# Kernel optimization log

Measured on AMD Instinct MI355X. Metric: run time of the kernel, lower is better.

## Reference

```python
import jax, jax.numpy as jnp
import numpy as np

B, S_IMG, S_TXT, D, H, HD = 1, 2048, 512, 3072, 24, 128
EMB, N_IP = 4096, 64
IP_SCALE = 1.0
EPS = 1e-6
SM_SCALE = 1.0 / np.sqrt(HD).astype(np.float32)


def _lin(x, W, b=None):
    # torch Linear: y = x @ W.T + b, W: [out, in]
    y = jnp.einsum('bsd,od->bso', x, W)
    return y if b is None else y + b


def _heads(x):  # [B,S,D] -> [B,H,S,HD]
    return x.reshape(B, -1, H, HD).transpose(0, 2, 1, 3)


def _rms(x, w):
    return x * jax.lax.rsqrt(jnp.mean(x * x, axis=-1, keepdims=True) + EPS) * w


def _rope(x, cos, sin):
    # interleaved real/imag rotation, cos/sin: [S, HD] broadcast over B,H
    xr = x.reshape(*x.shape[:-1], HD // 2, 2)
    rot = jnp.stack([-xr[..., 1], xr[..., 0]], axis=-1).reshape(x.shape)
    return x * cos + rot * sin


def _sdpa(q, k, v):
    s = jnp.einsum('bhqd,bhkd->bhqk', q, k) * SM_SCALE
    p = jax.nn.softmax(s, axis=-1)
    return jnp.einsum('bhqk,bhkd->bhqd', p, v)


def setup_inputs() -> dict:
    key = jax.random.key(0)
    ks = jax.random.split(key, 32)
    r = lambda i, shape: jax.random.normal(ks[i], shape, dtype=jnp.float32)
    w = lambda i, shape: r(i, shape) * 0.02
    inp = {
        'hidden_states': r(0, (B, S_IMG, D)),
        'encoder_hidden_states': r(1, (B, S_TXT, D)),
        'image_embeds': r(2, (B, N_IP, EMB)),
        'rope_cos': jnp.cos(r(3, (S_TXT + S_IMG, HD))),
        'rope_sin': jnp.sin(r(3, (S_TXT + S_IMG, HD))),
        'Wq': w(4, (D, D)), 'bq': jnp.zeros((D,)),
        'Wk': w(5, (D, D)), 'bk': jnp.zeros((D,)),
        'Wv': w(6, (D, D)), 'bv': jnp.zeros((D,)),
        'Waq': w(7, (D, D)), 'baq': jnp.zeros((D,)),
        'Wak': w(8, (D, D)), 'bak': jnp.zeros((D,)),
        'Wav': w(9, (D, D)), 'bav': jnp.zeros((D,)),
        'Wo': w(10, (D, D)), 'bo': jnp.zeros((D,)),
        'Wao': w(11, (D, D)), 'bao': jnp.zeros((D,)),
        'norm_q_w': jnp.ones((HD,)), 'norm_k_w': jnp.ones((HD,)),
        'norm_aq_w': jnp.ones((HD,)), 'norm_ak_w': jnp.ones((HD,)),
        'Wk_ip': w(12, (D, EMB)), 'Wv_ip': w(13, (D, EMB)),
        'txt_seq_len': S_TXT,
    }
    return inp


def reference(hidden_states, encoder_hidden_states, image_embeds, rope_cos, rope_sin,
              Wq, bq, Wk, bk, Wv, bv, Waq, baq, Wak, bak, Wav, bav,
              Wo, bo, Wao, bao, norm_q_w, norm_k_w, norm_aq_w, norm_ak_w,
              Wk_ip, Wv_ip, txt_seq_len):
    # main stream projections + per-head RMSNorm
    q = _rms(_heads(_lin(hidden_states, Wq, bq)), norm_q_w)
    k = _rms(_heads(_lin(hidden_states, Wk, bk)), norm_k_w)
    v = _heads(_lin(hidden_states, Wv, bv))
    # encoder (text) stream projections + RMSNorm, concat text before image
    eq = _rms(_heads(_lin(encoder_hidden_states, Waq, baq)), norm_aq_w)
    ek = _rms(_heads(_lin(encoder_hidden_states, Wak, bak)), norm_ak_w)
    ev = _heads(_lin(encoder_hidden_states, Wav, bav))
    q = jnp.concatenate([eq, q], axis=2)
    k = jnp.concatenate([ek, k], axis=2)
    v = jnp.concatenate([ev, v], axis=2)
    # IP-adapter branch uses pre-RoPE image-token queries
    ip_q = q[:, :, txt_seq_len:]
    ip_k = _heads(_lin(image_embeds, Wk_ip))
    ip_v = _heads(_lin(image_embeds, Wv_ip))
    ip_hs = _sdpa(ip_q, ip_k, ip_v).transpose(0, 2, 1, 3).reshape(B, -1, H * HD)
    # rotary on joint q/k, then main attention
    q = _rope(q, rope_cos, rope_sin)
    k = _rope(k, rope_cos, rope_sin)
    hs = _sdpa(q, k, v).transpose(0, 2, 1, 3).reshape(B, -1, H * HD)
    # add scaled IP-adapter output to the image part
    img = hs[:, txt_seq_len:] + IP_SCALE * ip_hs
    enc = hs[:, :txt_seq_len]
    # output projections
    out_img = _lin(img, Wo, bo)
    out_enc = _lin(enc, Wao, bao)
    return out_img, out_enc
```

## Files before the change

### kernel.cpp

```cpp
#include <hip/hip_runtime.h>
#include <hip/hip_bf16.h>

#define H 24
#define HD 128
#define DMODEL 3072
#define S_IMG 2048
#define S_TXT 512
#define S_ALL 2560
#define EMB 4096
#define N_IP 64
#define SM_SCALE 0.08838834764831845f

typedef __attribute__((ext_vector_type(8))) short short8;
typedef __attribute__((ext_vector_type(4))) float f32x4;
typedef __attribute__((ext_vector_type(16))) float f32x16;

__device__ inline unsigned short f2bf(float f) {
    unsigned u = __builtin_bit_cast(unsigned, f);
    return (unsigned short)((u + 0x7fffu + ((u >> 16) & 1u)) >> 16);
}
__device__ inline unsigned pk2(float a, float b) {
    return (unsigned)f2bf(a) | ((unsigned)f2bf(b) << 16);
}
__device__ inline float bf2f(unsigned short u) {
    unsigned x = ((unsigned)u) << 16;
    return __builtin_bit_cast(float, x);
}

__device__ inline void gload16(const void* g, void* l) {
    __builtin_amdgcn_global_load_lds(
        (const __attribute__((address_space(1))) unsigned int*)g,
        (__attribute__((address_space(3))) unsigned int*)(unsigned int)(unsigned long long)l,
        16, 0, 0);
}

struct CastSegs {
    const float* src[13];
    unsigned short* dst[13];
    int n8[13];
    int ntot8[13];
    int bstart[14];
};

__global__ __launch_bounds__(256)
void castall(CastSegs cs)
{
    int b = blockIdx.x, seg = 0;
    while (seg < 12 && b >= cs.bstart[seg + 1]) seg++;
    int nb = cs.bstart[seg + 1] - cs.bstart[seg];
    int lb = b - cs.bstart[seg];
    const float* in = cs.src[seg];
    unsigned short* out = cs.dst[seg];
    int n8 = cs.n8[seg], ntot = cs.ntot8[seg];
    for (int i = lb * 256 + threadIdx.x; i < ntot; i += nb * 256) {
        int4 o;
        if (i < n8) {
            const float4* p = (const float4*)(in + (size_t)i * 8);
            float4 a = p[0], bb = p[1];
            o.x = pk2(a.x, a.y); o.y = pk2(a.z, a.w);
            o.z = pk2(bb.x, bb.y); o.w = pk2(bb.z, bb.w);
        } else {
            o.x = 0; o.y = 0; o.z = 0; o.w = 0;
        }
        *(int4*)(out + (size_t)i * 8) = o;
    }
}

__global__ __launch_bounds__(256)
void bcat2(const float* __restrict__ q0, const float* __restrict__ k0, const float* __restrict__ v0,
           const float* __restrict__ q1, const float* __restrict__ k1, const float* __restrict__ v1,
           float* __restrict__ d0, float* __restrict__ d1)
{
    int i = blockIdx.x * 256 + threadIdx.x;
    int which = i >= 3 * DMODEL;
    int j = which ? i - 3 * DMODEL : i;
    const float* a = which ? q1 : q0;
    const float* b = which ? k1 : k0;
    const float* c = which ? v1 : v0;
    float v = (j < DMODEL) ? a[j] : ((j < 2 * DMODEL) ? b[j - DMODEL] : c[j - 2 * DMODEL]);
    (which ? d1 : d0)[j] = v;
}

template<int OUTBF>
__global__ __launch_bounds__(256)
void gemmx(const unsigned short* __restrict__ A0, const unsigned short* __restrict__ B0,
           const float* __restrict__ b0, void* __restrict__ C0,
           const unsigned short* __restrict__ A1, const unsigned short* __restrict__ B1,
           const float* __restrict__ b1, void* __restrict__ C1,
           int mbSplit, int N, int K, int nbm, int GN)
{
    __shared__ unsigned short sm[2 * 8192];
    const int tid = threadIdx.x, lane = tid & 63, wid = tid >> 6;
    const int wr = wid >> 1, wc = wid & 1;
    const int r15 = lane & 15, g = lane >> 4;

    int nwg = gridDim.x;
    int t = (blockIdx.x & 7) * (nwg >> 3) + (blockIdx.x >> 3);
    int gsz = nbm * GN;
    int G = t / gsz, l = t - G * gsz;
    int mb = l % nbm, nb = G * GN + l / nbm;

    const unsigned short* A; const unsigned short* B; const float* bias; void* C; int mrow;
    if (mb < mbSplit) { A = A0; B = B0; bias = b0; C = C0; mrow = mb; }
    else             { A = A1; B = B1; bias = b1; C = C1; mrow = mb - mbSplit; }
    const int m0 = mrow * 128, n0 = nb * 128;

    const int lr = lane >> 3;
    const int lc = lane & 7;
    const int gcol = ((lc * 16) ^ (lr << 4)) >> 1;

    const unsigned short* Ab = A + (size_t)(m0 + wid * 32 + lr) * K + gcol;
    const unsigned short* Bb = B + (size_t)(n0 + wid * 32 + lr) * K + gcol;
    char* smc = (char*)sm;

    f32x4 acc[4][4];
    #pragma unroll
    for (int i = 0; i < 4; i++)
        #pragma unroll
        for (int j = 0; j < 4; j++)
            acc[i][j] = {0.f, 0.f, 0.f, 0.f};

    for (int k0 = 0; k0 < K; k0 += 64) {
        #pragma unroll
        for (int cc = 0; cc < 4; cc++) {
            gload16(Ab + (size_t)cc * 8 * K + k0, smc + (wid * 32 + cc * 8) * 128);
            gload16(Bb + (size_t)cc * 8 * K + k0, smc + 16384 + (wid * 32 + cc * 8) * 128);
        }
        __syncthreads();
        #pragma unroll
        for (int ks = 0; ks < 2; ks++) {
            short8 af[4], bf[4];
            #pragma unroll
            for (int mi = 0; mi < 4; mi++) {
                int row = wr * 64 + mi * 16 + r15;
                af[mi] = *(const short8*)(smc + row * 128 + ((ks * 64 + g * 16) ^ ((row & 7) << 4)));
            }
            #pragma unroll
            for (int ni = 0; ni < 4; ni++) {
                int row = wc * 64 + ni * 16 + r15;
                bf[ni] = *(const short8*)(smc + 16384 + row * 128 + ((ks * 64 + g * 16) ^ ((row & 7) << 4)));
            }
            #pragma unroll
            for (int mi = 0; mi < 4; mi++)
                #pragma unroll
                for (int ni = 0; ni < 4; ni++)
                    acc[mi][ni] = __builtin_amdgcn_mfma_f32_16x16x32_bf16(af[mi], bf[ni], acc[mi][ni], 0, 0, 0);
        }
        __syncthreads();
    }
    #pragma unroll
    for (int mi = 0; mi < 4; mi++) {
        #pragma unroll
        for (int ni = 0; ni < 4; ni++) {
            int col = n0 + wc * 64 + ni * 16 + r15;
            float bv = bias ? bias[col] : 0.f;
            #pragma unroll
            for (int r = 0; r < 4; r++) {
                int grow = m0 + wr * 64 + mi * 16 + g * 4 + r;
                float v = acc[mi][ni][r] + bv;
                if (OUTBF)
                    ((unsigned short*)C)[(size_t)grow * N + col] = f2bf(v);
                else
                    ((float*)C)[(size_t)grow * N + col] = v;
            }
        }
    }
}

__global__ __launch_bounds__(256)
void rmsropeQK(const unsigned short* __restrict__ qkvb,
               const float* __restrict__ nqw, const float* __restrict__ nkw,
               const float* __restrict__ naqw, const float* __restrict__ nakw,
               const float* __restrict__ cosb, const float* __restrict__ sinb,
               unsigned short* __restrict__ qb, unsigned short* __restrict__ kb,
               unsigned short* __restrict__ ipq)
{
    int wg = blockIdx.x * 4 + (threadIdx.x >> 6);
    int lane = threadIdx.x & 63;
    int s = wg / H, h = wg - s * H;
    const unsigned short* row = qkvb + (size_t)s * (3 * DMODEL);
    unsigned uq = *(const unsigned*)(row + h * HD + lane * 2);
    unsigned uk = *(const unsigned*)(row + DMODEL + h * HD + lane * 2);
    float q0 = bf2f((unsigned short)uq), q1 = bf2f((unsigned short)(uq >> 16));
    float k0 = bf2f((unsigned short)uk), k1 = bf2f((unsigned short)(uk >> 16));
    float sq = q0 * q0 + q1 * q1, sk = k0 * k0 + k1 * k1;
    #pragma unroll
    for (int off = 1; off < 64; off <<= 1) {
        sq += __shfl_xor(sq, off);
        sk += __shfl_xor(sk, off);
    }
    float rq = rsqrtf(sq * (1.f / HD) + 1e-6f) * SM_SCALE;
    float rk = rsqrtf(sk * (1.f / HD) + 1e-6f);
    const float* wq = (s < S_TXT) ? naqw : nqw;
    const float* wk = (s < S_TXT) ? nakw : nkw;
    float xq0 = q0 * rq * wq[lane * 2], xq1 = q1 * rq * wq[lane * 2 + 1];
    float xk0 = k0 * rk * wk[lane * 2], xk1 = k1 * rk * wk[lane * 2 + 1];
    if (s >= S_TXT)
        *(unsigned*)(ipq + (size_t)h * S_IMG * HD + (size_t)(s - S_TXT) * HD + lane * 2) = pk2(xq0, xq1);
    float c0 = cosb[s * HD + lane * 2], c1 = cosb[s * HD + lane * 2 + 1];
    float s0 = sinb[s * HD + lane * 2], s1 = sinb[s * HD + lane * 2 + 1];
    *(unsigned*)(qb + (size_t)h * S_ALL * HD + (size_t)s * HD + lane * 2) =
        pk2(xq0 * c0 - xq1 * s0, xq1 * c1 + xq0 * s1);
    *(unsigned*)(kb + (size_t)h * S_ALL * HD + (size_t)s * HD + lane * 2) =
        pk2(xk0 * c0 - xk1 * s0, xk1 * c1 + xk0 * s1);
}

__global__ __launch_bounds__(256)
void vtrans(const unsigned short* __restrict__ src, int stride,
            unsigned short* __restrict__ vt, int Stot)
{
    __shared__ unsigned short lv[64 * 130];
    int h = blockIdx.y;
    int s0 = blockIdx.x * 64;
    const unsigned short* base = src + (size_t)s0 * stride + h * HD;
    int tid = threadIdx.x;
    #pragma unroll
    for (int i = 0; i < 4; i++) {
        int slot = tid + 256 * i;
        int row = slot >> 4, c = slot & 15;
        int4 v = *(const int4*)(base + (size_t)row * stride + c * 8);
        unsigned* p = (unsigned*)(lv + row * 130 + c * 8);
        p[0] = (unsigned)v.x; p[1] = (unsigned)v.y; p[2] = (unsigned)v.z; p[3] = (unsigned)v.w;
    }
    __syncthreads();
    #pragma unroll
    for (int i = 0; i < 4; i++) {
        int slot = tid + 256 * i;
        int d = slot >> 3, c8 = slot & 7;
        unsigned w0 = lv[(c8 * 8 + 0) * 130 + d] | ((unsigned)lv[(c8 * 8 + 1) * 130 + d] << 16);
        unsigned w1 = lv[(c8 * 8 + 2) * 130 + d] | ((unsigned)lv[(c8 * 8 + 3) * 130 + d] << 16);
        unsigned w2 = lv[(c8 * 8 + 4) * 130 + d] | ((unsigned)lv[(c8 * 8 + 5) * 130 + d] << 16);
        unsigned w3 = lv[(c8 * 8 + 6) * 130 + d] | ((unsigned)lv[(c8 * 8 + 7) * 130 + d] << 16);
        int4 o = {(int)w0, (int)w1, (int)w2, (int)w3};
        *(int4*)(vt + (size_t)(h * HD + d) * Stot + s0 + c8 * 8) = o;
    }
}

__global__ __launch_bounds__(256)
void cast_heads8(const unsigned short* __restrict__ in, unsigned short* __restrict__ out)
{
    int idx = blockIdx.x * 256 + threadIdx.x;
    int s = idx / 384;
    int rem = idx - s * 384;
    int h = rem >> 4, d8 = rem & 15;
    int4 v = *(const int4*)(in + (size_t)s * (2 * DMODEL) + h * HD + d8 * 8);
    *(int4*)(out + ((size_t)h * N_IP + s) * HD + d8 * 8) = v;
}

template<int MODE, int KVBLK>
__global__ __launch_bounds__(512, 2)
void flash4(const unsigned short* __restrict__ Q, const unsigned short* __restrict__ Kb,
            const unsigned short* __restrict__ Vt, const unsigned short* __restrict__ ipb,
            unsigned short* __restrict__ Out, int Sq, int Skv)
{
    __shared__ char sm[66560];
    const int h = blockIdx.y;
    const int q0 = blockIdx.x * 256;
    const int tid = threadIdx.x, w = tid >> 6, lane = tid & 63;
    const int l31 = lane & 31, hi = lane >> 5;
    const int T2 = KVBLK / 32, K4 = KVBLK / 16, SLOTV = KVBLK / 8, NL = KVBLK / 32;
    const int VROWB = KVBLK * 2;

    const unsigned short* Qh = Q + ((size_t)h * Sq + q0 + w * 32 + l31) * HD + hi * 8;
    short8 qf[8];
    #pragma unroll
    for (int c = 0; c < 8; c++)
        qf[c] = *(const short8*)(Qh + c * 16);

    float m = -3.0e38f, lsum = 0.f;
    f32x16 o[4];
    #pragma unroll
    for (int dn = 0; dn < 4; dn++)
        #pragma unroll
        for (int r = 0; r < 16; r++) o[dn][r] = 0.f;

    const unsigned short* Kh = Kb + (size_t)h * Skv * HD;
    const unsigned short* Vth = Vt + (size_t)h * HD * Skv;
    float* scl = (float*)(sm + 65536) + w * 32;
    const int nt = Skv / KVBLK;

    for (int t = 0; t < nt; t++) {
        int kv0 = t * KVBLK;
        #pragma unroll
        for (int cc = 0; cc < NL; cc++) {
            int f = cc * 512 + tid;
            int row = f >> 4, slot = f & 15;
            gload16(Kh + (size_t)(kv0 + row) * HD + (((slot * 16) ^ ((row & 7) << 4)) >> 1),
                    sm + f * 16);
        }
        #pragma unroll
        for (int cc = 0; cc < NL; cc++) {
            int f = cc * 512 + tid;
            int d = f / SLOTV, slot = f % SLOTV;
            gload16(Vth + (size_t)d * Skv + kv0 + (((slot * 16) ^ ((d & 7) << 4)) >> 1),
                    sm + 32768 + f * 16);
        }
        __syncthreads();

        f32x16 st[T2];
        __builtin_amdgcn_s_setprio(1);
        #pragma unroll
        for (int t2 = 0; t2 < T2; t2++) {
            #pragma unroll
            for (int r = 0; r < 16; r++) st[t2][r] = 0.f;
            #pragma unroll
            for (int c = 0; c < 8; c++) {
                int krow = t2 * 32 + l31;
                short8 kf = *(const short8*)(sm + krow * 256 + ((c * 32 + hi * 16) ^ ((krow & 7) << 4)));
                st[t2] = __builtin_amdgcn_mfma_f32_32x32x16_bf16(kf, qf[c], st[t2], 0, 0, 0);
            }
        }
        __builtin_amdgcn_s_setprio(0);

        float pmax = st[0][0];
        #pragma unroll
        for (int t2 = 0; t2 < T2; t2++)
            #pragma unroll
            for (int r = 0; r < 16; r++) pmax = fmaxf(pmax, st[t2][r]);
        pmax = fmaxf(pmax, __shfl_xor(pmax, 32));

        if (!__all(pmax - m <= 8.0f)) {
            float mn = fmaxf(m, pmax);
            float sc = __expf(m - mn);
            m = mn;
            lsum *= sc;
            if (hi == 0) scl[l31] = sc;
            float scb[16];
            #pragma unroll
            for (int r = 0; r < 16; r++)
                scb[r] = scl[(r & 3) + 8 * (r >> 2) + 4 * hi];
            #pragma unroll
            for (int dn = 0; dn < 4; dn++)
                #pragma unroll
                for (int r = 0; r < 16; r++) o[dn][r] *= scb[r];
        }

        float psum = 0.f;
        #pragma unroll
        for (int t2 = 0; t2 < T2; t2++)
            #pragma unroll
            for (int r = 0; r < 16; r++) {
                float p = __expf(st[t2][r] - m);
                st[t2][r] = p;
                psum += p;
            }
        psum += __shfl_xor(psum, 32);
        lsum += psum;

        short8 pa[K4];
        #pragma unroll
        for (int k4 = 0; k4 < K4; k4++) {
            unsigned U  = pk2(st[(k4 * 8 + 0) >> 4][(k4 * 8 + 0) & 15], st[(k4 * 8 + 1) >> 4][(k4 * 8 + 1) & 15]);
            unsigned V  = pk2(st[(k4 * 8 + 2) >> 4][(k4 * 8 + 2) & 15], st[(k4 * 8 + 3) >> 4][(k4 * 8 + 3) & 15]);
            unsigned U2 = pk2(st[(k4 * 8 + 4) >> 4][(k4 * 8 + 4) & 15], st[(k4 * 8 + 5) >> 4][(k4 * 8 + 5) & 15]);
            unsigned V2 = pk2(st[(k4 * 8 + 6) >> 4][(k4 * 8 + 6) & 15], st[(k4 * 8 + 7) >> 4][(k4 * 8 + 7) & 15]);
            unsigned SU = __shfl_xor(U, 32), SU2 = __shfl_xor(U2, 32);
            unsigned SV = __shfl_xor(V, 32), SV2 = __shfl_xor(V2, 32);
            uint4 wv;
            wv.x = hi ? SU2 : U;
            wv.y = hi ? SV2 : V;
            wv.z = hi ? U2 : SU;
            wv.w = hi ? V2 : SV;
            pa[k4] = __builtin_bit_cast(short8, wv);
        }

        __builtin_amdgcn_s_setprio(1);
        #pragma unroll
        for (int dn = 0; dn < 4; dn++) {
            #pragma unroll
            for (int k4 = 0; k4 < K4; k4++) {
                int vrow = dn * 32 + l31;
                short8 vf = *(const short8*)(sm + 32768 + vrow * VROWB + ((k4 * 32 + hi * 16) ^ ((vrow & 7) << 4)));
                o[dn] = __builtin_amdgcn_mfma_f32_32x32x16_bf16(pa[k4], vf, o[dn], 0, 0, 0);
            }
        }
        __builtin_amdgcn_s_setprio(0);
        __syncthreads();
    }

    if (hi == 0) scl[l31] = 1.f / lsum;
    float linv[16];
    #pragma unroll
    for (int r = 0; r < 16; r++)
        linv[r] = scl[(r & 3) + 8 * (r >> 2) + 4 * hi];
    #pragma unroll
    for (int dn = 0; dn < 4; dn++) {
        #pragma unroll
        for (int r = 0; r < 16; r++) {
            int qrow = q0 + w * 32 + (r & 3) + 8 * (r >> 2) + 4 * hi;
            int col = h * HD + dn * 32 + l31;
            float val = o[dn][r] * linv[r];
            if (MODE == 1 && qrow >= S_TXT)
                val += bf2f(ipb[(size_t)(qrow - S_TXT) * DMODEL + col]);
            Out[(size_t)qrow * DMODEL + col] = f2bf(val);
        }
    }
}

extern "C" void kernel_launch(void* const* d_in, const int* in_sizes, int n_in,
                              void* d_out, int out_size, void* d_ws, size_t ws_size,
                              hipStream_t stream)
{
    const float* hs   = (const float*)d_in[0];
    const float* enc  = (const float*)d_in[1];
    const float* iemb = (const float*)d_in[2];
    const float* cosb = (const float*)d_in[3];
    const float* sinb = (const float*)d_in[4];
    const float* Wq  = (const float*)d_in[5];  const float* bq  = (const float*)d_in[6];
    const float* Wk  = (const float*)d_in[7];  const float* bk  = (const float*)d_in[8];
    const float* Wv  = (const float*)d_in[9];  const float* bv  = (const float*)d_in[10];
    const float* Waq = (const float*)d_in[11]; const float* baq = (const float*)d_in[12];
    const float* Wak = (const float*)d_in[13]; const float* bak = (const float*)d_in[14];
    const float* Wav = (const float*)d_in[15]; const float* bav = (const float*)d_in[16];
    const float* Wo  = (const float*)d_in[17]; const float* bo  = (const float*)d_in[18];
    const float* Wao = (const float*)d_in[19]; const float* bao = (const float*)d_in[20];
    const float* nq  = (const float*)d_in[21]; const float* nk  = (const float*)d_in[22];
    const float* naq = (const float*)d_in[23]; const float* nak = (const float*)d_in[24];
    const float* Wkip = (const float*)d_in[25]; const float* Wvip = (const float*)d_in[26];
    (void)in_sizes; (void)n_in; (void)out_size; (void)ws_size;

    char* ws = (char*)d_ws;
    size_t off = 0;
    auto alloc = [&](size_t b) { char* p = ws + off; off += (b + 255) & ~(size_t)255; return p; };
    unsigned short* qkvb    = (unsigned short*)alloc((size_t)S_ALL * 3 * DMODEL * 2);
    unsigned short* ipkvb   = (unsigned short*)alloc((size_t)128 * 2 * DMODEL * 2);
    unsigned short* hs_bf   = (unsigned short*)alloc((size_t)S_IMG * DMODEL * 2);
    unsigned short* enc_bf  = (unsigned short*)alloc((size_t)S_TXT * DMODEL * 2);
    unsigned short* iemb_bf = (unsigned short*)alloc((size_t)128 * EMB * 2);
    unsigned short* Wqkv  = (unsigned short*)alloc((size_t)3 * DMODEL * DMODEL * 2);
    unsigned short* Waqkv = (unsigned short*)alloc((size_t)3 * DMODEL * DMODEL * 2);
    unsigned short* Wo_b  = (unsigned short*)alloc((size_t)DMODEL * DMODEL * 2);
    unsigned short* Wao_b = (unsigned short*)alloc((size_t)DMODEL * DMODEL * 2);
    unsigned short* Wip   = (unsigned short*)alloc((size_t)2 * DMODEL * EMB * 2);
    float* bqkv  = (float*)alloc(3 * DMODEL * 4);
    float* baqkv = (float*)alloc(3 * DMODEL * 4);
    unsigned short* qb    = (unsigned short*)alloc((size_t)H * S_ALL * HD * 2);
    unsigned short* kbf   = (unsigned short*)alloc((size_t)H * S_ALL * HD * 2);
    unsigned short* vtb   = (unsigned short*)alloc((size_t)H * HD * S_ALL * 2);
    unsigned short* ipqb  = (unsigned short*)alloc((size_t)H * S_IMG * HD * 2);
    unsigned short* ipkb  = (unsigned short*)alloc((size_t)H * N_IP * HD * 2);
    unsigned short* ipvtb = (unsigned short*)alloc((size_t)H * HD * N_IP * 2);
    unsigned short* ipbuf = (unsigned short*)alloc((size_t)S_IMG * DMODEL * 2);
    unsigned short* attnb = (unsigned short*)alloc((size_t)S_ALL * DMODEL * 2);

    const size_t DD = (size_t)DMODEL * DMODEL;
    const size_t DE = (size_t)DMODEL * EMB;
    const int D8 = (int)(DD / 8), E8 = (int)(DE / 8);

    CastSegs cs;
    const float* srcs[13] = {hs, enc, iemb, Wq, Wk, Wv, Waq, Wak, Wav, Wo, Wao, Wkip, Wvip};
    unsigned short* dsts[13] = {hs_bf, enc_bf, iemb_bf,
                                Wqkv, Wqkv + DD, Wqkv + 2 * DD,
                                Waqkv, Waqkv + DD, Waqkv + 2 * DD,
                                Wo_b, Wao_b, Wip, Wip + DE};
    int n8s[13]  = {S_IMG * DMODEL / 8, S_TXT * DMODEL / 8, N_IP * EMB / 8,
                    D8, D8, D8, D8, D8, D8, D8, D8, E8, E8};
    int nt8s[13] = {S_IMG * DMODEL / 8, S_TXT * DMODEL / 8, 128 * EMB / 8,
                    D8, D8, D8, D8, D8, D8, D8, D8, E8, E8};
    int acc = 0;
    for (int i = 0; i < 13; i++) {
        cs.src[i] = srcs[i]; cs.dst[i] = dsts[i];
        cs.n8[i] = n8s[i]; cs.ntot8[i] = nt8s[i];
        cs.bstart[i] = acc;
        int nb = (nt8s[i] + 8191) / 8192;
        acc += (nb < 1 ? 1 : nb);
    }
    cs.bstart[13] = acc;

    dim3 blk(256);
    castall<<<dim3(acc), blk, 0, stream>>>(cs);
    bcat2<<<dim3(72), blk, 0, stream>>>(bq, bk, bv, baq, bak, bav, bqkv, baqkv);

    gemmx<1><<<dim3(20 * 72), blk, 0, stream>>>(
        hs_bf, Wqkv, bqkv, qkvb + (size_t)S_TXT * 3 * DMODEL,
        enc_bf, Waqkv, baqkv, qkvb,
        16, 3 * DMODEL, DMODEL, 20, 9);
    gemmx<1><<<dim3(48), blk, 0, stream>>>(
        iemb_bf, Wip, nullptr, ipkvb,
        iemb_bf, Wip, nullptr, ipkvb,
        1, 2 * DMODEL, EMB, 1, 6);

    rmsropeQK<<<dim3(15360), blk, 0, stream>>>(qkvb, nq, nk, naq, nak, cosb, sinb, qb, kbf, ipqb);
    vtrans<<<dim3(40, 24), blk, 0, stream>>>(qkvb + 2 * DMODEL, 3 * DMODEL, vtb, S_ALL);
    cast_heads8<<<dim3(96), blk, 0, stream>>>(ipkvb, ipkb);
    vtrans<<<dim3(1, 24), blk, 0, stream>>>(ipkvb + DMODEL, 2 * DMODEL, ipvtb, N_IP);

    dim3 fblk(512);
    flash4<0, 64><<<dim3(8, 24),  fblk, 0, stream>>>(ipqb, ipkb, ipvtb, nullptr, ipbuf, S_IMG, N_IP);
    flash4<1, 128><<<dim3(10, 24), fblk, 0, stream>>>(qb, kbf, vtb, ipbuf, attnb, S_ALL, S_ALL);

    float* dout = (float*)d_out;
    gemmx<0><<<dim3(20 * 24), blk, 0, stream>>>(
        attnb, Wao_b, bao, dout + (size_t)S_IMG * DMODEL,
        attnb + (size_t)S_TXT * DMODEL, Wo_b, bo, dout,
        4, DMODEL, DMODEL, 20, 3);
}
```

Baseline: 655.2 us.

## Add 256x128-tile 8-wave GEMM with triple-buffered LDS for QKV and output projections

Introduces gemm8, a 512-thread GEMM with 256x128 output tiles, a three-stage LDS ring filled by direct global-to-LDS loads, XOR-swizzled shared layout, and an XCD-aware block remapping. It replaces gemmx for the fused QKV projection and the output projections. The goal is better operand reuse per tile and better overlap of loads with MFMA. The trade-off is fewer workgroups (720 and 240), which risks under-filling the GPU on the smaller output GEMM, plus higher LDS use per block.

After: 639.2 us. -2.4%, faster.

```diff
diff --git a/kernel.cpp b/kernel.cpp
--- a/kernel.cpp
+++ b/kernel.cpp
@@ -157,6 +157,105 @@
             #pragma unroll
             for (int r = 0; r < 4; r++) {
                 int grow = m0 + wr * 64 + mi * 16 + g * 4 + r;
+                float v = acc[mi][ni][r] + bv;
+                if (OUTBF)
+                    ((unsigned short*)C)[(size_t)grow * N + col] = f2bf(v);
+                else
+                    ((float*)C)[(size_t)grow * N + col] = v;
+            }
+        }
+    }
+}
+
+template<int OUTBF>
+__global__ __launch_bounds__(512, 4)
+void gemm8(const unsigned short* __restrict__ A0, const unsigned short* __restrict__ B0,
+           const float* __restrict__ b0, void* __restrict__ C0,
+           const unsigned short* __restrict__ A1, const unsigned short* __restrict__ B1,
+           const float* __restrict__ b1, void* __restrict__ C1,
+           int mbSplit, int N, int K, int nbn)
+{
+    __shared__ char sm[73728];
+    const int tid = threadIdx.x, lane = tid & 63, wid = tid >> 6;
+    const int wm = wid >> 2, wn = wid & 3;
+    const int r15 = lane & 15, g = lane >> 4;
+
+    int nwg = gridDim.x;
+    int t0 = (blockIdx.x & 7) * (nwg >> 3) + (blockIdx.x >> 3);
+    int mb = t0 / nbn, nb = t0 - mb * nbn;
+
+    const unsigned short* A; const unsigned short* B; const float* bias; void* C; int mrow;
+    if (mb < mbSplit) { A = A0; B = B0; bias = b0; C = C0; mrow = mb; }
+    else              { A = A1; B = B1; bias = b1; C = C1; mrow = mb - mbSplit; }
+    const int m0 = mrow * 256, n0 = nb * 128;
+
+    const int fA0 = tid, fA1 = 512 + tid;
+    const int rA0 = fA0 >> 2, sA0 = fA0 & 3;
+    const int rA1 = fA1 >> 2, sA1 = fA1 & 3;
+    const int rB = tid >> 2, sB = tid & 3;
+    const unsigned short* Asrc0 = A + (size_t)(m0 + rA0) * K + ((sA0 ^ (rA0 & 3)) << 3);
+    const unsigned short* Asrc1 = A + (size_t)(m0 + rA1) * K + ((sA1 ^ (rA1 & 3)) << 3);
+    const unsigned short* Bsrc  = B + (size_t)(n0 + rB) * K + ((sB ^ (rB & 3)) << 3);
+
+    f32x4 acc[8][2];
+    #pragma unroll
+    for (int i = 0; i < 8; i++)
+        #pragma unroll
+        for (int j = 0; j < 2; j++)
+            acc[i][j] = {0.f, 0.f, 0.f, 0.f};
+
+    const int nt = K >> 5;
+
+    auto STAGE = [&](int buf, int kt) {
+        char* d = sm + buf * 24576;
+        gload16(Asrc0 + (kt << 5), d + fA0 * 16);
+        gload16(Asrc1 + (kt << 5), d + fA1 * 16);
+        gload16(Bsrc  + (kt << 5), d + 16384 + tid * 16);
+    };
+
+    STAGE(0, 0);
+    STAGE(1, 1);
+    asm volatile("s_waitcnt vmcnt(3)" ::: "memory");
+    __builtin_amdgcn_s_barrier();
+
+    int cur = 0, nxt = 2;
+    for (int t = 0; t < nt; t++) {
+        if (t + 2 < nt) STAGE(nxt, t + 2);
+        const char* As = sm + cur * 24576;
+        const char* Bs = As + 16384;
+        short8 bfr[2];
+        #pragma unroll
+        for (int ni = 0; ni < 2; ni++) {
+            int brow = wn * 32 + ni * 16 + r15;
+            bfr[ni] = *(const short8*)(Bs + brow * 64 + ((g ^ (brow & 3)) << 4));
+        }
+        __builtin_amdgcn_s_setprio(1);
+        #pragma unroll
+        for (int mi = 0; mi < 8; mi++) {
+            int arow = wm * 128 + mi * 16 + r15;
+            short8 af = *(const short8*)(As + arow * 64 + ((g ^ (arow & 3)) << 4));
+            acc[mi][0] = __builtin_amdgcn_mfma_f32_16x16x32_bf16(af, bfr[0], acc[mi][0], 0, 0, 0);
+            acc[mi][1] = __builtin_amdgcn_mfma_f32_16x16x32_bf16(af, bfr[1], acc[mi][1], 0, 0, 0);
+        }
+        __builtin_amdgcn_s_setprio(0);
+        if (t + 1 < nt) {
+            if (t + 2 < nt) { asm volatile("s_waitcnt vmcnt(3)" ::: "memory"); }
+            else            { asm volatile("s_waitcnt vmcnt(0)" ::: "memory"); }
+            __builtin_amdgcn_s_barrier();
+        }
+        cur = (cur == 2) ? 0 : cur + 1;
+        nxt = (nxt == 2) ? 0 : nxt + 1;
+    }
+
+    #pragma unroll
+    for (int mi = 0; mi < 8; mi++) {
+        #pragma unroll
+        for (int ni = 0; ni < 2; ni++) {
+            int col = n0 + wn * 32 + ni * 16 + r15;
+            float bv = bias ? bias[col] : 0.f;
+            #pragma unroll
+            for (int r = 0; r < 4; r++) {
+                int grow = m0 + wm * 128 + mi * 16 + g * 4 + r;
                 float v = acc[mi][ni][r] + bv;
                 if (OUTBF)
                     ((unsigned short*)C)[(size_t)grow * N + col] = f2bf(v);
@@ -471,10 +570,10 @@
     castall<<<dim3(acc), blk, 0, stream>>>(cs);
     bcat2<<<dim3(72), blk, 0, stream>>>(bq, bk, bv, baq, bak, bav, bqkv, baqkv);
 
-    gemmx<1><<<dim3(20 * 72), blk, 0, stream>>>(
+    gemm8<1><<<dim3(720), dim3(512), 0, stream>>>(
         hs_bf, Wqkv, bqkv, qkvb + (size_t)S_TXT * 3 * DMODEL,
         enc_bf, Waqkv, baqkv, qkvb,
-        16, 3 * DMODEL, DMODEL, 20, 9);
+        8, 3 * DMODEL, DMODEL, 72);
     gemmx<1><<<dim3(48), blk, 0, stream>>>(
         iemb_bf, Wip, nullptr, ipkvb,
         iemb_bf, Wip, nullptr, ipkvb,
@@ -490,8 +589,8 @@
     flash4<1, 128><<<dim3(10, 24), fblk, 0, stream>>>(qb, kbf, vtb, ipbuf, attnb, S_ALL, S_ALL);
 
     float* dout = (float*)d_out;
-    gemmx<0><<<dim3(20 * 24), blk, 0, stream>>>(
+    gemm8<0><<<dim3(240), dim3(512), 0, stream>>>(
+        attnb + (size_t)S_TXT * DMODEL, Wo_b, bo, dout,
         attnb, Wao_b, bao, dout + (size_t)S_IMG * DMODEL,
-        attnb + (size_t)S_TXT * DMODEL, Wo_b, bo, dout,
-        4, DMODEL, DMODEL, 20, 3);
-}
+        8, DMODEL, DMODEL, 24);
+}
```

## Replace GEMM with triple-buffered 256x128 kernel fusing IP GEMM and weight casts

Applied to the files above, without the earlier changes.

Replaces the two-buffer-free 128x128 GEMM with a 512-thread 256x128 tile kernel that uses a three-stage LDS pipeline with vmcnt waits and s_setprio around MFMA. The QKV, text QKV and IP-adapter K/V projections now run in a single launch, and spare blocks cast Wo/Wao to bf16 there instead of in the cast kernel. The flash kernels get an XCD-aware 1D block swizzle. This is meant to cut launch count and global-load stalls in the GEMMs, at the cost of more LDS per block and padded work for the IP GEMM (256-row tiles over 64 real rows).

After: 622.4 us. -5.0%, faster.

```diff
diff --git a/kernel.cpp b/kernel.cpp
--- a/kernel.cpp
+++ b/kernel.cpp
@@ -81,37 +81,62 @@
     (which ? d1 : d0)[j] = v;
 }
 
+struct GSet {
+    const unsigned short* A;
+    const unsigned short* B;
+    const float* bias;
+    void* C;
+    int N, K, nbn;
+};
+
 template<int OUTBF>
-__global__ __launch_bounds__(256)
-void gemmx(const unsigned short* __restrict__ A0, const unsigned short* __restrict__ B0,
-           const float* __restrict__ b0, void* __restrict__ C0,
-           const unsigned short* __restrict__ A1, const unsigned short* __restrict__ B1,
-           const float* __restrict__ b1, void* __restrict__ C1,
-           int mbSplit, int N, int K, int nbm, int GN)
-{
-    __shared__ unsigned short sm[2 * 8192];
+__global__ __launch_bounds__(512, 4)
+void gemm8(GSet s0, GSet s1, GSet s2, int e0, int e1, int e2,
+           const float* cs0, unsigned short* cd0,
+           const float* cs1, unsigned short* cd1, int cn8)
+{
+    __shared__ char sm[73728];
     const int tid = threadIdx.x, lane = tid & 63, wid = tid >> 6;
-    const int wr = wid >> 1, wc = wid & 1;
+    const int wm = wid >> 1, wn = wid & 1;
     const int r15 = lane & 15, g = lane >> 4;
 
     int nwg = gridDim.x;
-    int t = (blockIdx.x & 7) * (nwg >> 3) + (blockIdx.x >> 3);
-    int gsz = nbm * GN;
-    int G = t / gsz, l = t - G * gsz;
-    int mb = l % nbm, nb = G * GN + l / nbm;
-
-    const unsigned short* A; const unsigned short* B; const float* bias; void* C; int mrow;
-    if (mb < mbSplit) { A = A0; B = B0; bias = b0; C = C0; mrow = mb; }
-    else             { A = A1; B = B1; bias = b1; C = C1; mrow = mb - mbSplit; }
-    const int m0 = mrow * 128, n0 = nb * 128;
-
-    const int lr = lane >> 3;
-    const int lc = lane & 7;
-    const int gcol = ((lc * 16) ^ (lr << 4)) >> 1;
-
-    const unsigned short* Ab = A + (size_t)(m0 + wid * 32 + lr) * K + gcol;
-    const unsigned short* Bb = B + (size_t)(n0 + wid * 32 + lr) * K + gcol;
-    char* smc = (char*)sm;
+    int t0 = (blockIdx.x & 7) * (nwg >> 3) + (blockIdx.x >> 3);
+
+    if (t0 >= e2) {
+        int lb = t0 - e2;
+        const float* src = (lb >> 4) ? cs1 : cs0;
+        unsigned short* dst = (lb >> 4) ? cd1 : cd0;
+        int b = lb & 15;
+        for (int i = b * 512 + tid; i < cn8; i += 16 * 512) {
+            const float4* p = (const float4*)(src + (size_t)i * 8);
+            float4 a = p[0], bb = p[1];
+            int4 o;
+            o.x = pk2(a.x, a.y); o.y = pk2(a.z, a.w);
+            o.z = pk2(bb.x, bb.y); o.w = pk2(bb.z, bb.w);
+            *(int4*)(dst + (size_t)i * 8) = o;
+        }
+        return;
+    }
+
+    GSet S; int local;
+    if (t0 < e0)      { S = s0; local = t0; }
+    else if (t0 < e1) { S = s1; local = t0 - e0; }
+    else              { S = s2; local = t0 - e1; }
+    const int mb = local / S.nbn, nb = local - mb * S.nbn;
+    const int m0 = mb * 256, n0 = nb * 128;
+    const int K = S.K, N = S.N;
+    const unsigned short* A = S.A;
+    const unsigned short* B = S.B;
+    const float* bias = S.bias;
+
+    const int fA0 = tid, fA1 = 512 + tid;
+    const int rA0 = fA0 >> 2, sA0 = fA0 & 3;
+    const int rA1 = fA1 >> 2, sA1 = fA1 & 3;
+    const int rB = tid >> 2, sB = tid & 3;
+    const unsigned short* Asrc0 = A + (size_t)(m0 + rA0) * K + ((sA0 ^ ((rA0 >> 1) & 3)) << 3);
+    const unsigned short* Asrc1 = A + (size_t)(m0 + rA1) * K + ((sA1 ^ ((rA1 >> 1) & 3)) << 3);
+    const unsigned short* Bsrc  = B + (size_t)(n0 + rB) * K + ((sB ^ ((rB >> 1) & 3)) << 3);
 
     f32x4 acc[4][4];
     #pragma unroll
@@ -120,48 +145,64 @@
         for (int j = 0; j < 4; j++)
             acc[i][j] = {0.f, 0.f, 0.f, 0.f};
 
-    for (int k0 = 0; k0 < K; k0 += 64) {
-        #pragma unroll
-        for (int cc = 0; cc < 4; cc++) {
-            gload16(Ab + (size_t)cc * 8 * K + k0, smc + (wid * 32 + cc * 8) * 128);
-            gload16(Bb + (size_t)cc * 8 * K + k0, smc + 16384 + (wid * 32 + cc * 8) * 128);
-        }
-        __syncthreads();
-        #pragma unroll
-        for (int ks = 0; ks < 2; ks++) {
-            short8 af[4], bf[4];
-            #pragma unroll
-            for (int mi = 0; mi < 4; mi++) {
-                int row = wr * 64 + mi * 16 + r15;
-                af[mi] = *(const short8*)(smc + row * 128 + ((ks * 64 + g * 16) ^ ((row & 7) << 4)));
-            }
-            #pragma unroll
-            for (int ni = 0; ni < 4; ni++) {
-                int row = wc * 64 + ni * 16 + r15;
-                bf[ni] = *(const short8*)(smc + 16384 + row * 128 + ((ks * 64 + g * 16) ^ ((row & 7) << 4)));
-            }
-            #pragma unroll
-            for (int mi = 0; mi < 4; mi++)
-                #pragma unroll
-                for (int ni = 0; ni < 4; ni++)
-                    acc[mi][ni] = __builtin_amdgcn_mfma_f32_16x16x32_bf16(af[mi], bf[ni], acc[mi][ni], 0, 0, 0);
-        }
-        __syncthreads();
-    }
+    const int nt = K >> 5;
+
+    auto STAGE = [&](int buf, int kt) {
+        char* d = sm + buf * 24576;
+        gload16(Asrc0 + (kt << 5), d + fA0 * 16);
+        gload16(Asrc1 + (kt << 5), d + fA1 * 16);
+        gload16(Bsrc  + (kt << 5), d + 16384 + tid * 16);
+    };
+
+    STAGE(0, 0);
+    STAGE(1, 1);
+    asm volatile("s_waitcnt vmcnt(3)" ::: "memory");
+    __builtin_amdgcn_s_barrier();
+
+    int cur = 0, nxt = 2;
+    for (int t = 0; t < nt; t++) {
+        if (t + 2 < nt) STAGE(nxt, t + 2);
+        const char* As = sm + cur * 24576;
+        const char* Bs = As + 16384;
+        short8 bfr[4];
+        #pragma unroll
+        for (int ni = 0; ni < 4; ni++) {
+            int brow = wn * 64 + ni * 16 + r15;
+            bfr[ni] = *(const short8*)(Bs + brow * 64 + ((g ^ ((brow >> 1) & 3)) << 4));
+        }
+        __builtin_amdgcn_s_setprio(1);
+        #pragma unroll
+        for (int mi = 0; mi < 4; mi++) {
+            int arow = wm * 64 + mi * 16 + r15;
+            short8 af = *(const short8*)(As + arow * 64 + ((g ^ ((arow >> 1) & 3)) << 4));
+            #pragma unroll
+            for (int ni = 0; ni < 4; ni++)
+                acc[mi][ni] = __builtin_amdgcn_mfma_f32_16x16x32_bf16(af, bfr[ni], acc[mi][ni], 0, 0, 0);
+        }
+        __builtin_amdgcn_s_setprio(0);
+        if (t + 1 < nt) {
+            if (t + 2 < nt) { asm volatile("s_waitcnt vmcnt(3)" ::: "memory"); }
+            else            { asm volatile("s_waitcnt vmcnt(0)" ::: "memory"); }
+            __builtin_amdgcn_s_barrier();
+        }
+        cur = (cur == 2) ? 0 : cur + 1;
+        nxt = (nxt == 2) ? 0 : nxt + 1;
+    }
+
     #pragma unroll
     for (int mi = 0; mi < 4; mi++) {
         #pragma unroll
         for (int ni = 0; ni < 4; ni++) {
-            int col = n0 + wc * 64 + ni * 16 + r15;
+            int col = n0 + wn * 64 + ni * 16 + r15;
             float bv = bias ? bias[col] : 0.f;
             #pragma unroll
             for (int r = 0; r < 4; r++) {
-                int grow = m0 + wr * 64 + mi * 16 + g * 4 + r;
+                int grow = m0 + wm * 64 + mi * 16 + g * 4 + r;
                 float v = acc[mi][ni][r] + bv;
                 if (OUTBF)
-                    ((unsigned short*)C)[(size_t)grow * N + col] = f2bf(v);
+                    ((unsigned short*)S.C)[(size_t)grow * N + col] = f2bf(v);
                 else
-                    ((float*)C)[(size_t)grow * N + col] = v;
+                    ((float*)S.C)[(size_t)grow * N + col] = v;
             }
         }
     }
@@ -247,15 +288,17 @@
     *(int4*)(out + ((size_t)h * N_IP + s) * HD + d8 * 8) = v;
 }
 
-template<int MODE, int KVBLK>
+template<int MODE, int KVBLK, int NQB>
 __global__ __launch_bounds__(512, 2)
 void flash4(const unsigned short* __restrict__ Q, const unsigned short* __restrict__ Kb,
             const unsigned short* __restrict__ Vt, const unsigned short* __restrict__ ipb,
             unsigned short* __restrict__ Out, int Sq, int Skv)
 {
     __shared__ char sm[66560];
-    const int h = blockIdx.y;
-    const int q0 = blockIdx.x * 256;
+    int bid = blockIdx.x;
+    int gidx = (bid & 7) * (gridDim.x >> 3) + (bid >> 3);
+    const int h = gidx / NQB;
+    const int q0 = (gidx - h * NQB) * 256;
     const int tid = threadIdx.x, w = tid >> 6, lane = tid & 63;
     const int l31 = lane & 31, hi = lane >> 5;
     const int T2 = KVBLK / 32, K4 = KVBLK / 16, SLOTV = KVBLK / 8, NL = KVBLK / 32;
@@ -423,10 +466,10 @@
     size_t off = 0;
     auto alloc = [&](size_t b) { char* p = ws + off; off += (b + 255) & ~(size_t)255; return p; };
     unsigned short* qkvb    = (unsigned short*)alloc((size_t)S_ALL * 3 * DMODEL * 2);
-    unsigned short* ipkvb   = (unsigned short*)alloc((size_t)128 * 2 * DMODEL * 2);
+    unsigned short* ipkvb   = (unsigned short*)alloc((size_t)256 * 2 * DMODEL * 2);
     unsigned short* hs_bf   = (unsigned short*)alloc((size_t)S_IMG * DMODEL * 2);
     unsigned short* enc_bf  = (unsigned short*)alloc((size_t)S_TXT * DMODEL * 2);
-    unsigned short* iemb_bf = (unsigned short*)alloc((size_t)128 * EMB * 2);
+    unsigned short* iemb_bf = (unsigned short*)alloc((size_t)256 * EMB * 2);
     unsigned short* Wqkv  = (unsigned short*)alloc((size_t)3 * DMODEL * DMODEL * 2);
     unsigned short* Waqkv = (unsigned short*)alloc((size_t)3 * DMODEL * DMODEL * 2);
     unsigned short* Wo_b  = (unsigned short*)alloc((size_t)DMODEL * DMODEL * 2);
@@ -448,37 +491,35 @@
     const int D8 = (int)(DD / 8), E8 = (int)(DE / 8);
 
     CastSegs cs;
-    const float* srcs[13] = {hs, enc, iemb, Wq, Wk, Wv, Waq, Wak, Wav, Wo, Wao, Wkip, Wvip};
-    unsigned short* dsts[13] = {hs_bf, enc_bf, iemb_bf,
+    const float* srcs[11] = {hs, enc, iemb, Wq, Wk, Wv, Waq, Wak, Wav, Wkip, Wvip};
+    unsigned short* dsts[11] = {hs_bf, enc_bf, iemb_bf,
                                 Wqkv, Wqkv + DD, Wqkv + 2 * DD,
                                 Waqkv, Waqkv + DD, Waqkv + 2 * DD,
-                                Wo_b, Wao_b, Wip, Wip + DE};
-    int n8s[13]  = {S_IMG * DMODEL / 8, S_TXT * DMODEL / 8, N_IP * EMB / 8,
-                    D8, D8, D8, D8, D8, D8, D8, D8, E8, E8};
-    int nt8s[13] = {S_IMG * DMODEL / 8, S_TXT * DMODEL / 8, 128 * EMB / 8,
-                    D8, D8, D8, D8, D8, D8, D8, D8, E8, E8};
+                                Wip, Wip + DE};
+    int n8s[11]  = {S_IMG * DMODEL / 8, S_TXT * DMODEL / 8, N_IP * EMB / 8,
+                    D8, D8, D8, D8, D8, D8, E8, E8};
+    int nt8s[11] = {S_IMG * DMODEL / 8, S_TXT * DMODEL / 8, 256 * EMB / 8,
+                    D8, D8, D8, D8, D8, D8, E8, E8};
     int acc = 0;
-    for (int i = 0; i < 13; i++) {
+    for (int i = 0; i < 11; i++) {
         cs.src[i] = srcs[i]; cs.dst[i] = dsts[i];
         cs.n8[i] = n8s[i]; cs.ntot8[i] = nt8s[i];
         cs.bstart[i] = acc;
         int nb = (nt8s[i] + 8191) / 8192;
         acc += (nb < 1 ? 1 : nb);
     }
-    cs.bstart[13] = acc;
+    for (int i = 11; i < 14; i++) cs.bstart[i] = acc;
 
     dim3 blk(256);
     castall<<<dim3(acc), blk, 0, stream>>>(cs);
     bcat2<<<dim3(72), blk, 0, stream>>>(bq, bk, bv, baq, bak, bav, bqkv, baqkv);
 
-    gemmx<1><<<dim3(20 * 72), blk, 0, stream>>>(
-        hs_bf, Wqkv, bqkv, qkvb + (size_t)S_TXT * 3 * DMODEL,
-        enc_bf, Waqkv, baqkv, qkvb,
-        16, 3 * DMODEL, DMODEL, 20, 9);
-    gemmx<1><<<dim3(48), blk, 0, stream>>>(
-        iemb_bf, Wip, nullptr, ipkvb,
-        iemb_bf, Wip, nullptr, ipkvb,
-        1, 2 * DMODEL, EMB, 1, 6);
+    GSet sImg = {hs_bf,  Wqkv,  bqkv,  qkvb + (size_t)S_TXT * 3 * DMODEL, 3 * DMODEL, DMODEL, 72};
+    GSet sTxt = {enc_bf, Waqkv, baqkv, qkvb,                              3 * DMODEL, DMODEL, 72};
+    GSet sIp  = {iemb_bf, Wip,  nullptr, ipkvb,                           2 * DMODEL, EMB,    48};
+    gemm8<1><<<dim3(800), dim3(512), 0, stream>>>(
+        sImg, sTxt, sIp, 576, 720, 768,
+        Wo, Wo_b, Wao, Wao_b, D8);
 
     rmsropeQK<<<dim3(15360), blk, 0, stream>>>(qkvb, nq, nk, naq, nak, cosb, sinb, qb, kbf, ipqb);
     vtrans<<<dim3(40, 24), blk, 0, stream>>>(qkvb + 2 * DMODEL, 3 * DMODEL, vtb, S_ALL);
@@ -486,12 +527,12 @@
     vtrans<<<dim3(1, 24), blk, 0, stream>>>(ipkvb + DMODEL, 2 * DMODEL, ipvtb, N_IP);
 
     dim3 fblk(512);
-    flash4<0, 64><<<dim3(8, 24),  fblk, 0, stream>>>(ipqb, ipkb, ipvtb, nullptr, ipbuf, S_IMG, N_IP);
-    flash4<1, 128><<<dim3(10, 24), fblk, 0, stream>>>(qb, kbf, vtb, ipbuf, attnb, S_ALL, S_ALL);
-
-    float* dout = (float*)d_out;
-    gemmx<0><<<dim3(20 * 24), blk, 0, stream>>>(
-        attnb, Wao_b, bao, dout + (size_t)S_IMG * DMODEL,
-        attnb + (size_t)S_TXT * DMODEL, Wo_b, bo, dout,
-        4, DMODEL, DMODEL, 20, 3);
-}
+    flash4<0, 64, 8><<<dim3(192), fblk, 0, stream>>>(ipqb, ipkb, ipvtb, nullptr, ipbuf, S_IMG, N_IP);
+    flash4<1, 128, 10><<<dim3(240), fblk, 0, stream>>>(qb, kbf, vtb, ipbuf, attnb, S_ALL, S_ALL);
+
+    GSet oImg = {attnb + (size_t)S_TXT * DMODEL, Wo_b,  bo,  d_out,                                DMODEL, DMODEL, 24};
+    GSet oTxt = {attnb,                          Wao_b, bao, (float*)d_out + (size_t)S_IMG * DMODEL, DMODEL, DMODEL, 24};
+    gemm8<0><<<dim3(240), dim3(512), 0, stream>>>(
+        oImg, oTxt, oTxt, 192, 240, 240,
+        nullptr, nullptr, nullptr, nullptr, 0);
+}
```
